# Kernel optimization log

Hardware: AMD Instinct MI355X
Metric: run time of the kernel (lower is better)

## Reference

```python
import jax, jax.numpy as jnp
import numpy as np

QUERY_DIM, FEAT_DIM, HID_DIM, OUT_DIM = 512, 2048, 512, 512
B, L, S, T = 8, 128, 100, 100


def setup_inputs() -> dict:
    key = jax.random.key(0)
    ks = jax.random.split(key, 9)
    d = {
        "query": jax.random.normal(ks[0], (B, L, QUERY_DIM), jnp.float32),
        "src": jax.random.normal(ks[1], (B, S, FEAT_DIM), jnp.float32),
        "trg": jax.random.normal(ks[2], (B, T, FEAT_DIM), jnp.float32),
        # params (LinearAct == Linear + identity act); src/trg projections share weights
        "Wq": jax.random.normal(ks[3], (QUERY_DIM, HID_DIM), jnp.float32) / np.sqrt(QUERY_DIM),
        "bq": jnp.zeros((HID_DIM,), jnp.float32),
        "Ws": jax.random.normal(ks[4], (FEAT_DIM, HID_DIM), jnp.float32) / np.sqrt(FEAT_DIM),
        "bs": jnp.zeros((HID_DIM,), jnp.float32),
        "Wo": jax.random.normal(ks[5], (HID_DIM + QUERY_DIM, OUT_DIM), jnp.float32) / np.sqrt(HID_DIM + QUERY_DIM),
        "bo": jnp.zeros((OUT_DIM,), jnp.float32),
    }
    return d


def reference(query, src, trg, Wq, bq, Ws, bs, Wo, bo):
    b, l, _ = query.shape
    s = src.shape[1]
    t = trg.shape[1]
    q = query @ Wq + bq          # b,l,k
    s_key = src @ Ws + bs        # b,s,k
    t_key = trg @ Ws + bs        # b,t,k
    hid = q.shape[-1]
    # score[b,l,s,t] = q . (s_key - t_key)/sqrt(2) / sqrt(hid) -- decomposed, no b,s,t,k tensor
    qs = jnp.einsum('blk,bsk->bls', q, s_key)
    qt = jnp.einsum('blk,btk->blt', q, t_key)
    score = (qs[:, :, :, None] - qt[:, :, None, :]) / jnp.sqrt(jnp.asarray(2.0 * hid, q.dtype))
    w = jax.nn.softmax(score.reshape(b, l, s * t), axis=-1).reshape(b, l, s, t)
    # ctx = sum_{s,t} w * (s_key - t_key)/sqrt(2), decomposed via marginals
    ws = w.sum(axis=3)           # b,l,s
    wt = w.sum(axis=2)           # b,l,t
    ctx = (jnp.einsum('bls,bsk->blk', ws, s_key) - jnp.einsum('blt,btk->blk', wt, t_key)) / jnp.sqrt(jnp.asarray(2.0, q.dtype))
    x = jnp.concatenate([query, ctx], axis=-1) @ Wo + bo
    return x
```

## Files before the change

### kernel.cpp

```cpp
#include <hip/hip_runtime.h>
#include <math.h>


typedef __attribute__((ext_vector_type(8))) short s16x8;
typedef __attribute__((ext_vector_type(4))) float f32x4;

__device__ __forceinline__ unsigned short f2bf(float f) {
    unsigned int u = __float_as_uint(f);
    return (unsigned short)((u + 0x7fffu + ((u >> 16) & 1u)) >> 16);
}

__device__ __forceinline__ s16x8 cvt8(const float* p) {
    float4 u = *(const float4*)p, w = *(const float4*)(p + 4);
    s16x8 o;
    o[0] = (short)f2bf(u.x); o[1] = (short)f2bf(u.y);
    o[2] = (short)f2bf(u.z); o[3] = (short)f2bf(u.w);
    o[4] = (short)f2bf(w.x); o[5] = (short)f2bf(w.y);
    o[6] = (short)f2bf(w.z); o[7] = (short)f2bf(w.w);
    return o;
}

__global__ __launch_bounds__(256) void k_prep(
    const float* __restrict__ Wq, const float* __restrict__ Ws,
    const float* __restrict__ Wo,
    unsigned short* __restrict__ WqT, unsigned short* __restrict__ WsT,
    unsigned short* __restrict__ WoT) {
    __shared__ float tile[32][33];
    const int id = blockIdx.x, t = threadIdx.x;

    const float* W; unsigned short* O; int K, tk, tn;
    if (id < 256)       { W = Wq; O = WqT; K = 512;  tk = id >> 4;          tn = id & 15; }
    else if (id < 1280) { W = Ws; O = WsT; K = 2048; tk = (id - 256) >> 4;  tn = (id - 256) & 15; }
    else                { W = Wo; O = WoT; K = 1024; tk = (id - 1280) >> 4; tn = (id - 1280) & 15; }
    const int row = t >> 3, c4 = (t & 7) * 4;
    float4 v = *(const float4*)(W + (size_t)(tk * 32 + row) * 512 + tn * 32 + c4);
    tile[row][c4 + 0] = v.x; tile[row][c4 + 1] = v.y;
    tile[row][c4 + 2] = v.z; tile[row][c4 + 3] = v.w;
    __syncthreads();
    ushort4 o = make_ushort4(f2bf(tile[c4 + 0][row]), f2bf(tile[c4 + 1][row]),
                             f2bf(tile[c4 + 2][row]), f2bf(tile[c4 + 3][row]));
    *(ushort4*)(O + (size_t)(tn * 32 + row) * K + tk * 32 + c4) = o;
}

__device__ __forceinline__ void gemm64_keys(
    const float* __restrict__ src, const float* __restrict__ trg,
    const unsigned short* __restrict__ BT, unsigned short* __restrict__ Kb,
    int m0, int n0, unsigned short* As, unsigned short* Bs) {
    const int t = threadIdx.x;
    const int lane = t & 63, wid = t >> 6;
    const int wm = (wid & 1) * 32, wn = (wid >> 1) * 32;
    const int lr = lane & 15, lq = lane >> 4;
    const int r = t >> 3, c8 = (t & 7) * 8;

    const int ra_row = m0 + r, rb_row = m0 + r + 32;
    const float* arp = (ra_row < 800) ? (src + (size_t)ra_row * 2048)
                                      : (trg + (size_t)(ra_row - 800) * 2048);
    const float* brp = (rb_row < 800) ? (src + (size_t)rb_row * 2048)
                                      : (trg + (size_t)(rb_row - 800) * 2048);

    s16x8 ra0, ra1, rb0, rb1;
#define LDK(kt)                                                            \
    ra0 = cvt8(arp + (kt) + c8);                                           \
    ra1 = cvt8(brp + (kt) + c8);                                           \
    rb0 = *(const s16x8*)(BT + (size_t)(n0 + r)      * 2048 + (kt) + c8);  \
    rb1 = *(const s16x8*)(BT + (size_t)(n0 + r + 32) * 2048 + (kt) + c8);

    f32x4 acc[2][2] = {};
    LDK(0);
    for (int it = 0; it < 32; it++) {
        __syncthreads();
        *(s16x8*)&As[r * 72 + c8]        = ra0;
        *(s16x8*)&As[(r + 32) * 72 + c8] = ra1;
        *(s16x8*)&Bs[r * 72 + c8]        = rb0;
        *(s16x8*)&Bs[(r + 32) * 72 + c8] = rb1;
        __syncthreads();
        if (it < 31) { LDK((it + 1) * 64); }
#pragma unroll
        for (int s = 0; s < 2; s++) {
            s16x8 a0 = *(const s16x8*)&As[(wm + lr) * 72      + s * 32 + lq * 8];
            s16x8 a1 = *(const s16x8*)&As[(wm + 16 + lr) * 72 + s * 32 + lq * 8];
            s16x8 b0 = *(const s16x8*)&Bs[(wn + lr) * 72      + s * 32 + lq * 8];
            s16x8 b1 = *(const s16x8*)&Bs[(wn + 16 + lr) * 72 + s * 32 + lq * 8];
            acc[0][0] = __builtin_amdgcn_mfma_f32_16x16x32_bf16(a0, b0, acc[0][0], 0, 0, 0);
            acc[0][1] = __builtin_amdgcn_mfma_f32_16x16x32_bf16(a0, b1, acc[0][1], 0, 0, 0);
            acc[1][0] = __builtin_amdgcn_mfma_f32_16x16x32_bf16(a1, b0, acc[1][0], 0, 0, 0);
            acc[1][1] = __builtin_amdgcn_mfma_f32_16x16x32_bf16(a1, b1, acc[1][1], 0, 0, 0);
        }
    }
#undef LDK
#pragma unroll
    for (int i = 0; i < 2; i++)
#pragma unroll
        for (int j = 0; j < 2; j++) {
            const int col = n0 + wn + j * 16 + lr;
            const int row = m0 + wm + i * 16 + lq * 4;
#pragma unroll
            for (int rr = 0; rr < 4; rr++)
                Kb[(size_t)(row + rr) * 512 + col] = f2bf(acc[i][j][rr]);
        }
}

__device__ __forceinline__ void gemm64_P(
    const unsigned short* __restrict__ Kb, const unsigned short* __restrict__ wotBot,
    float* __restrict__ P, int m0, int n0, unsigned short* As,
    unsigned short* Bs) {
    const int t = threadIdx.x;
    const int lane = t & 63, wid = t >> 6;
    const int wm = (wid & 1) * 32, wn = (wid >> 1) * 32;
    const int lr = lane & 15, lq = lane >> 4;
    const int r = t >> 3, c8 = (t & 7) * 8;

    s16x8 ra0, ra1, rb0, rb1;
#define LDP(kt)                                                               \
    ra0 = *(const s16x8*)(Kb + (size_t)(m0 + r)      * 512 + (kt) + c8);      \
    ra1 = *(const s16x8*)(Kb + (size_t)(m0 + r + 32) * 512 + (kt) + c8);      \
    rb0 = *(const s16x8*)(wotBot + (size_t)(n0 + r)      * 1024 + (kt) + c8); \
    rb1 = *(const s16x8*)(wotBot + (size_t)(n0 + r + 32) * 1024 + (kt) + c8);

    f32x4 acc[2][2] = {};
    LDP(0);
    for (int it = 0; it < 8; it++) {
        __syncthreads();
        *(s16x8*)&As[r * 72 + c8]        = ra0;
        *(s16x8*)&As[(r + 32) * 72 + c8] = ra1;
        *(s16x8*)&Bs[r * 72 + c8]        = rb0;
        *(s16x8*)&Bs[(r + 32) * 72 + c8] = rb1;
        __syncthreads();
        if (it < 7) { LDP((it + 1) * 64); }
#pragma unroll
        for (int s = 0; s < 2; s++) {
            s16x8 a0 = *(const s16x8*)&As[(wm + lr) * 72      + s * 32 + lq * 8];
            s16x8 a1 = *(const s16x8*)&As[(wm + 16 + lr) * 72 + s * 32 + lq * 8];
            s16x8 b0 = *(const s16x8*)&Bs[(wn + lr) * 72      + s * 32 + lq * 8];
            s16x8 b1 = *(const s16x8*)&Bs[(wn + 16 + lr) * 72 + s * 32 + lq * 8];
            acc[0][0] = __builtin_amdgcn_mfma_f32_16x16x32_bf16(a0, b0, acc[0][0], 0, 0, 0);
            acc[0][1] = __builtin_amdgcn_mfma_f32_16x16x32_bf16(a0, b1, acc[0][1], 0, 0, 0);
            acc[1][0] = __builtin_amdgcn_mfma_f32_16x16x32_bf16(a1, b0, acc[1][0], 0, 0, 0);
            acc[1][1] = __builtin_amdgcn_mfma_f32_16x16x32_bf16(a1, b1, acc[1][1], 0, 0, 0);
        }
    }
#undef LDP
#pragma unroll
    for (int i = 0; i < 2; i++)
#pragma unroll
        for (int j = 0; j < 2; j++) {
            const int col = n0 + wn + j * 16 + lr;
            const int row = m0 + wm + i * 16 + lq * 4;
#pragma unroll
            for (int rr = 0; rr < 4; rr++)
                P[(size_t)(row + rr) * 512 + col] = acc[i][j][rr];
        }
}

template <int MODE>
__device__ __forceinline__ void gemm32(
    const float* __restrict__ A, const unsigned short* __restrict__ BT,
    const float* __restrict__ bias, void* __restrict__ Cv,
    int m0, int n0, int KA, int KB, int N, int kiters,
    unsigned short* As, unsigned short* Bs) {
    const int t = threadIdx.x;
    const int lane = t & 63, wid = t >> 6;
    const int wm = (wid & 1) * 16, wn = (wid >> 1) * 32;
    const int lr = lane & 15, lq = lane >> 4;
    const int r = t >> 3, c8 = (t & 7) * 8;

    s16x8 ra, rb0, rb1;
#define LD32(kt)                                                            \
    ra  = cvt8(A + (size_t)(m0 + r) * KA + (kt) + c8);                      \
    rb0 = *(const s16x8*)(BT + (size_t)(n0 + r)      * KB + (kt) + c8);     \
    rb1 = *(const s16x8*)(BT + (size_t)(n0 + r + 32) * KB + (kt) + c8);

    f32x4 acc[2] = {};
    LD32(0);
    for (int it = 0; it < kiters; it++) {
        __syncthreads();
        *(s16x8*)&As[r * 72 + c8]        = ra;
        *(s16x8*)&Bs[r * 72 + c8]        = rb0;
        *(s16x8*)&Bs[(r + 32) * 72 + c8] = rb1;
        __syncthreads();
        if (it + 1 < kiters) { LD32((it + 1) * 64); }
#pragma unroll
        for (int s = 0; s < 2; s++) {
            s16x8 a0 = *(const s16x8*)&As[(wm + lr) * 72      + s * 32 + lq * 8];
            s16x8 b0 = *(const s16x8*)&Bs[(wn + lr) * 72      + s * 32 + lq * 8];
            s16x8 b1 = *(const s16x8*)&Bs[(wn + 16 + lr) * 72 + s * 32 + lq * 8];
            acc[0] = __builtin_amdgcn_mfma_f32_16x16x32_bf16(a0, b0, acc[0], 0, 0, 0);
            acc[1] = __builtin_amdgcn_mfma_f32_16x16x32_bf16(a0, b1, acc[1], 0, 0, 0);
        }
    }
#undef LD32
#pragma unroll
    for (int j = 0; j < 2; j++) {
        const int col = n0 + wn + j * 16 + lr;
        const int row = m0 + wm + lq * 4;
        const float bv = bias[col];
        if (MODE == 0) {
            float* C = (float*)Cv;
#pragma unroll
            for (int rr = 0; rr < 4; rr++)
                C[(size_t)(row + rr) * N + col] = acc[j][rr] + bv;
        } else {
            unsigned short* C = (unsigned short*)Cv;
#pragma unroll
            for (int rr = 0; rr < 4; rr++)
                C[(size_t)(row + rr) * N + col] = f2bf(acc[j][rr] + bv);
        }
    }
}

__global__ __launch_bounds__(256) void k_stageB(
    const float* __restrict__ query, const float* __restrict__ src,
    const float* __restrict__ trg, const unsigned short* __restrict__ WqT,
    const unsigned short* __restrict__ WsT, const unsigned short* __restrict__ WoT,
    const float* __restrict__ bq, const float* __restrict__ bo,
    unsigned short* __restrict__ qh, unsigned short* __restrict__ keysbf,
    float* __restrict__ out) {
    __shared__ __align__(16) unsigned short As[64 * 72];
    __shared__ __align__(16) unsigned short Bs[64 * 72];
    const int bid = blockIdx.x;
    if (bid < 200) {
        gemm64_keys(src, trg, WsT, keysbf, (bid >> 3) * 64, (bid & 7) * 64,
                    As, Bs);
    } else if (bid < 456) {
        const int r = bid - 200;
        gemm32<2>(query, WqT, bq, qh, (r >> 3) * 32, (r & 7) * 64, 512, 512,
                  512, 8, As, Bs);
    } else {
        const int r = bid - 456;
        gemm32<0>(query, WoT, bo, out, (r >> 3) * 32, (r & 7) * 64, 512, 1024,
                  512, 8, As, Bs);
    }
}

__global__ __launch_bounds__(256) void k_stageC(
    const unsigned short* __restrict__ qh, const unsigned short* __restrict__ keysbf,
    const unsigned short* __restrict__ wotBot, float* __restrict__ sc,
    float* __restrict__ P) {
    __shared__ __align__(16) unsigned short As[64 * 72];
    __shared__ __align__(16) unsigned short Bs[64 * 72];
    const int bid = blockIdx.x;
    const int t = threadIdx.x;

    if (bid >= 128) {
        const int rem = bid - 128;
        gemm64_P(keysbf, wotBot, P, (rem >> 3) * 64, (rem & 7) * 64, As, Bs);
        return;
    }

    const int mt = bid >> 2, nt = bid & 3;
    const int m0 = mt * 32, b = mt >> 2, n0 = nt * 64;
    const int lane = t & 63, wid = t >> 6;
    const int wm = (wid & 1) * 16, wn = (wid >> 1) * 32;
    const int lr = lane & 15, lq = lane >> 4;
    const int r = t >> 3, c8 = (t & 7) * 8;

    const int nA = n0 + r, nB = n0 + r + 32;
    int kr0 = (nA < 128) ? (b * 100 + nA) : (800 + b * 100 + (nA - 128));
    int kr1 = (nB < 128) ? (b * 100 + nB) : (800 + b * 100 + (nB - 128));
    kr0 = kr0 > 1599 ? 1599 : kr0;
    kr1 = kr1 > 1599 ? 1599 : kr1;

    s16x8 ra, rb0, rb1;
#define LDSC(kt)                                                        \
    ra  = *(const s16x8*)(qh + (size_t)(m0 + r) * 512 + (kt) + c8);     \
    rb0 = *(const s16x8*)(keysbf + (size_t)kr0 * 512 + (kt) + c8);      \
    rb1 = *(const s16x8*)(keysbf + (size_t)kr1 * 512 + (kt) + c8);

    f32x4 acc[2] = {};
    LDSC(0);
    for (int it = 0; it < 8; it++) {
        __syncthreads();
        *(s16x8*)&As[r * 72 + c8]        = ra;
        *(s16x8*)&Bs[r * 72 + c8]        = rb0;
        *(s16x8*)&Bs[(r + 32) * 72 + c8] = rb1;
        __syncthreads();
        if (it < 7) { LDSC((it + 1) * 64); }
#pragma unroll
        for (int s = 0; s < 2; s++) {
            s16x8 a0 = *(const s16x8*)&As[(wm + lr) * 72      + s * 32 + lq * 8];
            s16x8 b0 = *(const s16x8*)&Bs[(wn + lr) * 72      + s * 32 + lq * 8];
            s16x8 b1 = *(const s16x8*)&Bs[(wn + 16 + lr) * 72 + s * 32 + lq * 8];
            acc[0] = __builtin_amdgcn_mfma_f32_16x16x32_bf16(a0, b0, acc[0], 0, 0, 0);
            acc[1] = __builtin_amdgcn_mfma_f32_16x16x32_bf16(a0, b1, acc[1], 0, 0, 0);
        }
    }
#undef LDSC
#pragma unroll
    for (int j = 0; j < 2; j++) {
        const int col = n0 + wn + j * 16 + lr;
        const int row = m0 + wm + lq * 4;
        const float scale = (col >= 128) ? -(1.0f / 32.0f) : (1.0f / 32.0f);
#pragma unroll
        for (int rr = 0; rr < 4; rr++)
            sc[(size_t)(row + rr) * 256 + col] = acc[j][rr] * scale;
    }
}

__global__ __launch_bounds__(256) void k_stageD(
    const float* __restrict__ sc, const float* __restrict__ P,
    float* __restrict__ out) {
    __shared__ float wbuf[200 * 33];
    __shared__ float Bs[40 * 32];

    const int t = threadIdx.x;
    const int b = blockIdx.y;
    const int n0 = blockIdx.x * 32;
    const int l0 = blockIdx.z * 32;
    const int wave = t >> 6, lane = t & 63;

    for (int i = 0; i < 8; i++) {
        const int li = wave * 8 + i;
        const float4 v = *(const float4*)(
            sc + (size_t)(b * 128 + l0 + li) * 256 + lane * 4);
        const float vv[4] = {v.x, v.y, v.z, v.w};
        const int c0 = lane * 4;
        float mS = -1e30f, mT = -1e30f;
#pragma unroll
        for (int j = 0; j < 4; j++) {
            const int col = c0 + j;
            if (col < 100) mS = fmaxf(mS, vv[j]);
            if (col >= 128 && col < 228) mT = fmaxf(mT, vv[j]);
        }
#pragma unroll
        for (int off = 32; off > 0; off >>= 1) {
            mS = fmaxf(mS, __shfl_xor(mS, off));
            mT = fmaxf(mT, __shfl_xor(mT, off));
        }
        float eS[4], eT[4], sS = 0.f, sT = 0.f;
#pragma unroll
        for (int j = 0; j < 4; j++) {
            const int col = c0 + j;
            eS[j] = (col < 100) ? __expf(vv[j] - mS) : 0.f;
            eT[j] = (col >= 128 && col < 228) ? __expf(vv[j] - mT) : 0.f;
            sS += eS[j]; sT += eT[j];
        }
#pragma unroll
        for (int off = 32; off > 0; off >>= 1) {
            sS += __shfl_xor(sS, off);
            sT += __shfl_xor(sT, off);
        }
        const float iS = 1.f / sS, iT = 1.f / sT;
#pragma unroll
        for (int j = 0; j < 4; j++) {
            const int col = c0 + j;
            if (col < 100) wbuf[col * 33 + li] = eS[j] * iS;
            if (col >= 128 && col < 228)
                wbuf[(100 + col - 128) * 33 + li] = eT[j] * iT;
        }
    }
    __syncthreads();

    const int tx = t & 7, ty = t >> 3;
    float rB[5];
    auto loadB = [&](int kbase) {
#pragma unroll
        for (int e = 0; e < 5; e++) {
            const int idx = t + e * 256;
            const int k = idx >> 5, j = idx & 31;
            const int kk = kbase + k;
            rB[e] = (kk < 100)
                ?  P[(size_t)(b * 100 + kk) * 512 + n0 + j]
                : -P[(size_t)(800 + b * 100 + (kk - 100)) * 512 + n0 + j];
        }
    };

    float acc[4] = {};
    loadB(0);
    for (int c5 = 0; c5 < 5; c5++) {
        __syncthreads();
#pragma unroll
        for (int e = 0; e < 5; e++) {
            const int idx = t + e * 256;
            Bs[idx] = rB[e];
        }
        __syncthreads();
        if (c5 < 4) loadB((c5 + 1) * 40);
#pragma unroll 8
        for (int k = 0; k < 40; k++) {
            const float ar = wbuf[(c5 * 40 + k) * 33 + ty];
            float br[4];
            *(float4*)br = *(const float4*)&Bs[k * 32 + tx * 4];
#pragma unroll
            for (int j = 0; j < 4; j++) acc[j] = fmaf(ar, br[j], acc[j]);
        }
    }

    const float s2 = 0.70710678118654752f;
    const int m = b * 128 + l0 + ty;
#pragma unroll
    for (int j = 0; j < 4; j++)
        unsafeAtomicAdd(&out[(size_t)m * 512 + n0 + tx * 4 + j], acc[j] * s2);
}


extern "C" void kernel_launch(void* const* d_in, const int* in_sizes, int n_in,
                              void* d_out, int out_size, void* d_ws, size_t ws_size,
                              hipStream_t stream) {
    const float* query = (const float*)d_in[0];
    const float* src   = (const float*)d_in[1];
    const float* trg   = (const float*)d_in[2];
    const float* Wq    = (const float*)d_in[3];
    const float* bq    = (const float*)d_in[4];
    const float* Ws    = (const float*)d_in[5];
    const float* Wo    = (const float*)d_in[7];
    const float* bo    = (const float*)d_in[8];
    float* out = (float*)d_out;

    unsigned short* keysbf = (unsigned short*)d_ws;
    float* sc = (float*)(keysbf + 819200);
    float* P  = sc + 262144;
    unsigned short* qh  = (unsigned short*)(P + 819200);
    unsigned short* wqt = qh  + 524288;
    unsigned short* wst = wqt + 262144;
    unsigned short* wot = wst + 1048576;

    k_prep<<<1792, 256, 0, stream>>>(Wq, Ws, Wo, wqt, wst, wot);
    k_stageB<<<712, 256, 0, stream>>>(query, src, trg, wqt, wst, wot, bq, bo,
                                      qh, keysbf, out);
    k_stageC<<<328, 256, 0, stream>>>(qh, keysbf, wot + 512, sc, P);
    k_stageD<<<dim3(16, 8, 4), 256, 0, stream>>>(sc, P, out);
}
```

Before: 134.5 us.

## Fold Wq/Ws transpose-convert into GEMM loads and drop prep kernel

Removes the separate weight transpose/convert kernel for Wq and Ws. The keys and query GEMMs now read the fp32 weights directly with strided scalar loads and convert them to bf16 while staging into shared memory. The Wo transpose moves into the first stage as extra blocks, and the query@Wo_top GEMM moves to the second stage, so there is one fewer launch. The trade-off is uncoalesced column-strided loads of Ws (16 scalar loads per thread, repeated by every M-tile block) in place of a one-time transpose.

```diff
diff --git a/kernel.cpp b/kernel.cpp
--- a/kernel.cpp
+++ b/kernel.cpp
@@ -20,37 +20,16 @@
     return o;
 }
 
-__global__ __launch_bounds__(256) void k_prep(
-    const float* __restrict__ Wq, const float* __restrict__ Ws,
-    const float* __restrict__ Wo,
-    unsigned short* __restrict__ WqT, unsigned short* __restrict__ WsT,
-    unsigned short* __restrict__ WoT) {
-    __shared__ float tile[32][33];
-    const int id = blockIdx.x, t = threadIdx.x;
-
-    const float* W; unsigned short* O; int K, tk, tn;
-    if (id < 256)       { W = Wq; O = WqT; K = 512;  tk = id >> 4;          tn = id & 15; }
-    else if (id < 1280) { W = Ws; O = WsT; K = 2048; tk = (id - 256) >> 4;  tn = (id - 256) & 15; }
-    else                { W = Wo; O = WoT; K = 1024; tk = (id - 1280) >> 4; tn = (id - 1280) & 15; }
-    const int row = t >> 3, c4 = (t & 7) * 4;
-    float4 v = *(const float4*)(W + (size_t)(tk * 32 + row) * 512 + tn * 32 + c4);
-    tile[row][c4 + 0] = v.x; tile[row][c4 + 1] = v.y;
-    tile[row][c4 + 2] = v.z; tile[row][c4 + 3] = v.w;
-    __syncthreads();
-    ushort4 o = make_ushort4(f2bf(tile[c4 + 0][row]), f2bf(tile[c4 + 1][row]),
-                             f2bf(tile[c4 + 2][row]), f2bf(tile[c4 + 3][row]));
-    *(ushort4*)(O + (size_t)(tn * 32 + row) * K + tk * 32 + c4) = o;
-}
-
 __device__ __forceinline__ void gemm64_keys(
     const float* __restrict__ src, const float* __restrict__ trg,
-    const unsigned short* __restrict__ BT, unsigned short* __restrict__ Kb,
+    const float* __restrict__ Ws, unsigned short* __restrict__ Kb,
     int m0, int n0, unsigned short* As, unsigned short* Bs) {
     const int t = threadIdx.x;
     const int lane = t & 63, wid = t >> 6;
     const int wm = (wid & 1) * 32, wn = (wid >> 1) * 32;
     const int lr = lane & 15, lq = lane >> 4;
     const int r = t >> 3, c8 = (t & 7) * 8;
+    const int nrow = t >> 2, kc16 = (t & 3) * 16;
 
     const int ra_row = m0 + r, rb_row = m0 + r + 32;
     const float* arp = (ra_row < 800) ? (src + (size_t)ra_row * 2048)
@@ -58,12 +37,14 @@
     const float* brp = (rb_row < 800) ? (src + (size_t)rb_row * 2048)
                                       : (trg + (size_t)(rb_row - 800) * 2048);
 
-    s16x8 ra0, ra1, rb0, rb1;
-#define LDK(kt)                                                            \
-    ra0 = cvt8(arp + (kt) + c8);                                           \
-    ra1 = cvt8(brp + (kt) + c8);                                           \
-    rb0 = *(const s16x8*)(BT + (size_t)(n0 + r)      * 2048 + (kt) + c8);  \
-    rb1 = *(const s16x8*)(BT + (size_t)(n0 + r + 32) * 2048 + (kt) + c8);
+    s16x8 ra0, ra1;
+    float bw[16];
+#define LDK(kt)                                                              \
+    ra0 = cvt8(arp + (kt) + c8);                                             \
+    ra1 = cvt8(brp + (kt) + c8);                                             \
+    _Pragma("unroll")                                                        \
+    for (int j = 0; j < 16; j++)                                             \
+        bw[j] = Ws[(size_t)((kt) + kc16 + j) * 512 + n0 + nrow];
 
     f32x4 acc[2][2] = {};
     LDK(0);
@@ -71,8 +52,16 @@
         __syncthreads();
         *(s16x8*)&As[r * 72 + c8]        = ra0;
         *(s16x8*)&As[(r + 32) * 72 + c8] = ra1;
-        *(s16x8*)&Bs[r * 72 + c8]        = rb0;
-        *(s16x8*)&Bs[(r + 32) * 72 + c8] = rb1;
+        {
+            s16x8 bb0, bb1;
+#pragma unroll
+            for (int j = 0; j < 8; j++) {
+                bb0[j] = (short)f2bf(bw[j]);
+                bb1[j] = (short)f2bf(bw[8 + j]);
+            }
+            *(s16x8*)&Bs[nrow * 72 + kc16]     = bb0;
+            *(s16x8*)&Bs[nrow * 72 + kc16 + 8] = bb1;
+        }
         __syncthreads();
         if (it < 31) { LDK((it + 1) * 64); }
 #pragma unroll
@@ -100,6 +89,109 @@
         }
 }
 
+__device__ __forceinline__ void gemm32_rawB(
+    const float* __restrict__ A, const float* __restrict__ W,
+    const float* __restrict__ bias, unsigned short* __restrict__ C,
+    int m0, int n0, unsigned short* As, unsigned short* Bs) {
+    const int t = threadIdx.x;
+    const int lane = t & 63, wid = t >> 6;
+    const int wm = (wid & 1) * 16, wn = (wid >> 1) * 32;
+    const int lr = lane & 15, lq = lane >> 4;
+    const int r = t >> 3, c8 = (t & 7) * 8;
+    const int nrow = t >> 2, kc16 = (t & 3) * 16;
+
+    s16x8 ra;
+    float bw[16];
+#define LDQ(kt)                                                              \
+    ra = cvt8(A + (size_t)(m0 + r) * 512 + (kt) + c8);                       \
+    _Pragma("unroll")                                                        \
+    for (int j = 0; j < 16; j++)                                             \
+        bw[j] = W[(size_t)((kt) + kc16 + j) * 512 + n0 + nrow];
+
+    f32x4 acc[2] = {};
+    LDQ(0);
+    for (int it = 0; it < 8; it++) {
+        __syncthreads();
+        *(s16x8*)&As[r * 72 + c8] = ra;
+        {
+            s16x8 bb0, bb1;
+#pragma unroll
+            for (int j = 0; j < 8; j++) {
+                bb0[j] = (short)f2bf(bw[j]);
+                bb1[j] = (short)f2bf(bw[8 + j]);
+            }
+            *(s16x8*)&Bs[nrow * 72 + kc16]     = bb0;
+            *(s16x8*)&Bs[nrow * 72 + kc16 + 8] = bb1;
+        }
+        __syncthreads();
+        if (it < 7) { LDQ((it + 1) * 64); }
+#pragma unroll
+        for (int s = 0; s < 2; s++) {
+            s16x8 a0 = *(const s16x8*)&As[(wm + lr) * 72      + s * 32 + lq * 8];
+            s16x8 b0 = *(const s16x8*)&Bs[(wn + lr) * 72      + s * 32 + lq * 8];
+            s16x8 b1 = *(const s16x8*)&Bs[(wn + 16 + lr) * 72 + s * 32 + lq * 8];
+            acc[0] = __builtin_amdgcn_mfma_f32_16x16x32_bf16(a0, b0, acc[0], 0, 0, 0);
+            acc[1] = __builtin_amdgcn_mfma_f32_16x16x32_bf16(a0, b1, acc[1], 0, 0, 0);
+        }
+    }
+#undef LDQ
+#pragma unroll
+    for (int j = 0; j < 2; j++) {
+        const int col = n0 + wn + j * 16 + lr;
+        const int row = m0 + wm + lq * 4;
+        const float bv = bias[col];
+#pragma unroll
+        for (int rr = 0; rr < 4; rr++)
+            C[(size_t)(row + rr) * 512 + col] = f2bf(acc[j][rr] + bv);
+    }
+}
+
+__device__ __forceinline__ void gemm32_cvtA(
+    const float* __restrict__ A, const unsigned short* __restrict__ BT,
+    const float* __restrict__ bias, float* __restrict__ C,
+    int m0, int n0, int KB, unsigned short* As, unsigned short* Bs) {
+    const int t = threadIdx.x;
+    const int lane = t & 63, wid = t >> 6;
+    const int wm = (wid & 1) * 16, wn = (wid >> 1) * 32;
+    const int lr = lane & 15, lq = lane >> 4;
+    const int r = t >> 3, c8 = (t & 7) * 8;
+
+    s16x8 ra, rb0, rb1;
+#define LD32(kt)                                                            \
+    ra  = cvt8(A + (size_t)(m0 + r) * 512 + (kt) + c8);                     \
+    rb0 = *(const s16x8*)(BT + (size_t)(n0 + r)      * KB + (kt) + c8);     \
+    rb1 = *(const s16x8*)(BT + (size_t)(n0 + r + 32) * KB + (kt) + c8);
+
+    f32x4 acc[2] = {};
+    LD32(0);
+    for (int it = 0; it < 8; it++) {
+        __syncthreads();
+        *(s16x8*)&As[r * 72 + c8]        = ra;
+        *(s16x8*)&Bs[r * 72 + c8]        = rb0;
+        *(s16x8*)&Bs[(r + 32) * 72 + c8] = rb1;
+        __syncthreads();
+        if (it < 7) { LD32((it + 1) * 64); }
+#pragma unroll
+        for (int s = 0; s < 2; s++) {
+            s16x8 a0 = *(const s16x8*)&As[(wm + lr) * 72      + s * 32 + lq * 8];
+            s16x8 b0 = *(const s16x8*)&Bs[(wn + lr) * 72      + s * 32 + lq * 8];
+            s16x8 b1 = *(const s16x8*)&Bs[(wn + 16 + lr) * 72 + s * 32 + lq * 8];
+            acc[0] = __builtin_amdgcn_mfma_f32_16x16x32_bf16(a0, b0, acc[0], 0, 0, 0);
+            acc[1] = __builtin_amdgcn_mfma_f32_16x16x32_bf16(a0, b1, acc[1], 0, 0, 0);
+        }
+    }
+#undef LD32
+#pragma unroll
+    for (int j = 0; j < 2; j++) {
+        const int col = n0 + wn + j * 16 + lr;
+        const int row = m0 + wm + lq * 4;
+        const float bv = bias[col];
+#pragma unroll
+        for (int rr = 0; rr < 4; rr++)
+            C[(size_t)(row + rr) * 512 + col] = acc[j][rr] + bv;
+    }
+}
+
 __device__ __forceinline__ void gemm64_P(
     const unsigned short* __restrict__ Kb, const unsigned short* __restrict__ wotBot,
     float* __restrict__ P, int m0, int n0, unsigned short* As,
@@ -152,98 +244,56 @@
         }
 }
 
-template <int MODE>
-__device__ __forceinline__ void gemm32(
-    const float* __restrict__ A, const unsigned short* __restrict__ BT,
-    const float* __restrict__ bias, void* __restrict__ Cv,
-    int m0, int n0, int KA, int KB, int N, int kiters,
-    unsigned short* As, unsigned short* Bs) {
-    const int t = threadIdx.x;
-    const int lane = t & 63, wid = t >> 6;
-    const int wm = (wid & 1) * 16, wn = (wid >> 1) * 32;
-    const int lr = lane & 15, lq = lane >> 4;
-    const int r = t >> 3, c8 = (t & 7) * 8;
-
-    s16x8 ra, rb0, rb1;
-#define LD32(kt)                                                            \
-    ra  = cvt8(A + (size_t)(m0 + r) * KA + (kt) + c8);                      \
-    rb0 = *(const s16x8*)(BT + (size_t)(n0 + r)      * KB + (kt) + c8);     \
-    rb1 = *(const s16x8*)(BT + (size_t)(n0 + r + 32) * KB + (kt) + c8);
-
-    f32x4 acc[2] = {};
-    LD32(0);
-    for (int it = 0; it < kiters; it++) {
-        __syncthreads();
-        *(s16x8*)&As[r * 72 + c8]        = ra;
-        *(s16x8*)&Bs[r * 72 + c8]        = rb0;
-        *(s16x8*)&Bs[(r + 32) * 72 + c8] = rb1;
-        __syncthreads();
-        if (it + 1 < kiters) { LD32((it + 1) * 64); }
-#pragma unroll
-        for (int s = 0; s < 2; s++) {
-            s16x8 a0 = *(const s16x8*)&As[(wm + lr) * 72      + s * 32 + lq * 8];
-            s16x8 b0 = *(const s16x8*)&Bs[(wn + lr) * 72      + s * 32 + lq * 8];
-            s16x8 b1 = *(const s16x8*)&Bs[(wn + 16 + lr) * 72 + s * 32 + lq * 8];
-            acc[0] = __builtin_amdgcn_mfma_f32_16x16x32_bf16(a0, b0, acc[0], 0, 0, 0);
-            acc[1] = __builtin_amdgcn_mfma_f32_16x16x32_bf16(a0, b1, acc[1], 0, 0, 0);
-        }
-    }
-#undef LD32
-#pragma unroll
-    for (int j = 0; j < 2; j++) {
-        const int col = n0 + wn + j * 16 + lr;
-        const int row = m0 + wm + lq * 4;
-        const float bv = bias[col];
-        if (MODE == 0) {
-            float* C = (float*)Cv;
-#pragma unroll
-            for (int rr = 0; rr < 4; rr++)
-                C[(size_t)(row + rr) * N + col] = acc[j][rr] + bv;
-        } else {
-            unsigned short* C = (unsigned short*)Cv;
-#pragma unroll
-            for (int rr = 0; rr < 4; rr++)
-                C[(size_t)(row + rr) * N + col] = f2bf(acc[j][rr] + bv);
-        }
-    }
-}
-
-__global__ __launch_bounds__(256) void k_stageB(
+__global__ __launch_bounds__(256) void k_stage1(
     const float* __restrict__ query, const float* __restrict__ src,
-    const float* __restrict__ trg, const unsigned short* __restrict__ WqT,
-    const unsigned short* __restrict__ WsT, const unsigned short* __restrict__ WoT,
-    const float* __restrict__ bq, const float* __restrict__ bo,
-    unsigned short* __restrict__ qh, unsigned short* __restrict__ keysbf,
-    float* __restrict__ out) {
+    const float* __restrict__ trg, const float* __restrict__ Wq,
+    const float* __restrict__ Ws, const float* __restrict__ Wo,
+    const float* __restrict__ bq, unsigned short* __restrict__ qh,
+    unsigned short* __restrict__ keysbf, unsigned short* __restrict__ wot) {
+    __shared__ __align__(16) unsigned short As[64 * 72];
+    __shared__ __align__(16) unsigned short Bs[64 * 72];
+    const int bid = blockIdx.x, t = threadIdx.x;
+
+    if (bid < 200) {
+        gemm64_keys(src, trg, Ws, keysbf, (bid >> 3) * 64, (bid & 7) * 64,
+                    As, Bs);
+    } else if (bid < 456) {
+        const int rr = bid - 200;
+        gemm32_rawB(query, Wq, bq, qh, (rr >> 3) * 32, (rr & 7) * 64, As, Bs);
+    } else {
+        float (*tile)[33] = (float(*)[33])As;
+        const int id2 = bid - 456;
+        const int tk = id2 >> 4, tn = id2 & 15;
+        const int row = t >> 3, c4 = (t & 7) * 4;
+        float4 v = *(const float4*)(Wo + (size_t)(tk * 32 + row) * 512 + tn * 32 + c4);
+        tile[row][c4 + 0] = v.x; tile[row][c4 + 1] = v.y;
+        tile[row][c4 + 2] = v.z; tile[row][c4 + 3] = v.w;
+        __syncthreads();
+        ushort4 o = make_ushort4(f2bf(tile[c4 + 0][row]), f2bf(tile[c4 + 1][row]),
+                                 f2bf(tile[c4 + 2][row]), f2bf(tile[c4 + 3][row]));
+        *(ushort4*)(wot + (size_t)(tn * 32 + row) * 1024 + tk * 32 + c4) = o;
+    }
+}
+
+__global__ __launch_bounds__(256) void k_stage2(
+    const float* __restrict__ query, const unsigned short* __restrict__ qh,
+    const unsigned short* __restrict__ keysbf,
+    const unsigned short* __restrict__ wot, const float* __restrict__ bo,
+    float* __restrict__ sc, float* __restrict__ P, float* __restrict__ out) {
     __shared__ __align__(16) unsigned short As[64 * 72];
     __shared__ __align__(16) unsigned short Bs[64 * 72];
     const int bid = blockIdx.x;
-    if (bid < 200) {
-        gemm64_keys(src, trg, WsT, keysbf, (bid >> 3) * 64, (bid & 7) * 64,
+    const int t = threadIdx.x;
+
+    if (bid >= 328) {
+        const int rr = bid - 328;
+        gemm32_cvtA(query, wot, bo, out, (rr >> 3) * 32, (rr & 7) * 64, 1024,
                     As, Bs);
-    } else if (bid < 456) {
-        const int r = bid - 200;
-        gemm32<2>(query, WqT, bq, qh, (r >> 3) * 32, (r & 7) * 64, 512, 512,
-                  512, 8, As, Bs);
-    } else {
-        const int r = bid - 456;
-        gemm32<0>(query, WoT, bo, out, (r >> 3) * 32, (r & 7) * 64, 512, 1024,
-                  512, 8, As, Bs);
-    }
-}
-
-__global__ __launch_bounds__(256) void k_stageC(
-    const unsigned short* __restrict__ qh, const unsigned short* __restrict__ keysbf,
-    const unsigned short* __restrict__ wotBot, float* __restrict__ sc,
-    float* __restrict__ P) {
-    __shared__ __align__(16) unsigned short As[64 * 72];
-    __shared__ __align__(16) unsigned short Bs[64 * 72];
-    const int bid = blockIdx.x;
-    const int t = threadIdx.x;
-
+        return;
+    }
     if (bid >= 128) {
         const int rem = bid - 128;
-        gemm64_P(keysbf, wotBot, P, (rem >> 3) * 64, (rem & 7) * 64, As, Bs);
+        gemm64_P(keysbf, wot + 512, P, (rem >> 3) * 64, (rem & 7) * 64, As, Bs);
         return;
     }
 
@@ -410,13 +460,10 @@
     float* sc = (float*)(keysbf + 819200);
     float* P  = sc + 262144;
     unsigned short* qh  = (unsigned short*)(P + 819200);
-    unsigned short* wqt = qh  + 524288;
-    unsigned short* wst = wqt + 262144;
-    unsigned short* wot = wst + 1048576;
-
-    k_prep<<<1792, 256, 0, stream>>>(Wq, Ws, Wo, wqt, wst, wot);
-    k_stageB<<<712, 256, 0, stream>>>(query, src, trg, wqt, wst, wot, bq, bo,
-                                      qh, keysbf, out);
-    k_stageC<<<328, 256, 0, stream>>>(qh, keysbf, wot + 512, sc, P);
+    unsigned short* wot = qh + 524288;
+
+    k_stage1<<<968, 256, 0, stream>>>(query, src, trg, Wq, Ws, Wo, bq,
+                                      qh, keysbf, wot);
+    k_stage2<<<584, 256, 0, stream>>>(query, qh, keysbf, wot, bo, sc, P, out);
     k_stageD<<<dim3(16, 8, 4), 256, 0, stream>>>(sc, P, out);
 }
```

After: 153.4 us. 14.0% more time.

## Split-K the key projection GEMM with atomics and rebalance stage work

Applied to the files above, without the earlier changes.

The src/trg key projection (K=2048) is split four ways across blocks, with fp32 atomic accumulation into a keys buffer that is zeroed in the prep kernel. Keys are now stored in fp32 and converted to bf16 when loaded in stage C. The Wo transpose moves into stage B and the query@Wo output GEMM moves into stage C, so both stages get more parallel work. The costs are atomic traffic, twice the key storage bandwidth, and nondeterministic summation order.

```diff
diff --git a/kernel.cpp b/kernel.cpp
--- a/kernel.cpp
+++ b/kernel.cpp
@@ -22,30 +22,33 @@
 
 __global__ __launch_bounds__(256) void k_prep(
     const float* __restrict__ Wq, const float* __restrict__ Ws,
-    const float* __restrict__ Wo,
     unsigned short* __restrict__ WqT, unsigned short* __restrict__ WsT,
-    unsigned short* __restrict__ WoT) {
+    float* __restrict__ keys) {
     __shared__ float tile[32][33];
     const int id = blockIdx.x, t = threadIdx.x;
 
-    const float* W; unsigned short* O; int K, tk, tn;
-    if (id < 256)       { W = Wq; O = WqT; K = 512;  tk = id >> 4;          tn = id & 15; }
-    else if (id < 1280) { W = Ws; O = WsT; K = 2048; tk = (id - 256) >> 4;  tn = (id - 256) & 15; }
-    else                { W = Wo; O = WoT; K = 1024; tk = (id - 1280) >> 4; tn = (id - 1280) & 15; }
-    const int row = t >> 3, c4 = (t & 7) * 4;
-    float4 v = *(const float4*)(W + (size_t)(tk * 32 + row) * 512 + tn * 32 + c4);
-    tile[row][c4 + 0] = v.x; tile[row][c4 + 1] = v.y;
-    tile[row][c4 + 2] = v.z; tile[row][c4 + 3] = v.w;
-    __syncthreads();
-    ushort4 o = make_ushort4(f2bf(tile[c4 + 0][row]), f2bf(tile[c4 + 1][row]),
-                             f2bf(tile[c4 + 2][row]), f2bf(tile[c4 + 3][row]));
-    *(ushort4*)(O + (size_t)(tn * 32 + row) * K + tk * 32 + c4) = o;
+    if (id < 1280) {
+        const float* W; unsigned short* O; int K, tk, tn;
+        if (id < 256) { W = Wq; O = WqT; K = 512;  tk = id >> 4;         tn = id & 15; }
+        else          { W = Ws; O = WsT; K = 2048; tk = (id - 256) >> 4; tn = (id - 256) & 15; }
+        const int row = t >> 3, c4 = (t & 7) * 4;
+        float4 v = *(const float4*)(W + (size_t)(tk * 32 + row) * 512 + tn * 32 + c4);
+        tile[row][c4 + 0] = v.x; tile[row][c4 + 1] = v.y;
+        tile[row][c4 + 2] = v.z; tile[row][c4 + 3] = v.w;
+        __syncthreads();
+        ushort4 o = make_ushort4(f2bf(tile[c4 + 0][row]), f2bf(tile[c4 + 1][row]),
+                                 f2bf(tile[c4 + 2][row]), f2bf(tile[c4 + 3][row]));
+        *(ushort4*)(O + (size_t)(tn * 32 + row) * K + tk * 32 + c4) = o;
+    } else {
+        const int f = ((id - 1280) * 256 + t) * 4;
+        *(float4*)(keys + f) = make_float4(0.f, 0.f, 0.f, 0.f);
+    }
 }
 
 __device__ __forceinline__ void gemm64_keys(
     const float* __restrict__ src, const float* __restrict__ trg,
-    const unsigned short* __restrict__ BT, unsigned short* __restrict__ Kb,
-    int m0, int n0, unsigned short* As, unsigned short* Bs) {
+    const unsigned short* __restrict__ BT, float* __restrict__ Kf,
+    int m0, int n0, int kbase, unsigned short* As, unsigned short* Bs) {
     const int t = threadIdx.x;
     const int lane = t & 63, wid = t >> 6;
     const int wm = (wid & 1) * 32, wn = (wid >> 1) * 32;
@@ -66,15 +69,15 @@
     rb1 = *(const s16x8*)(BT + (size_t)(n0 + r + 32) * 2048 + (kt) + c8);
 
     f32x4 acc[2][2] = {};
-    LDK(0);
-    for (int it = 0; it < 32; it++) {
+    LDK(kbase);
+    for (int it = 0; it < 8; it++) {
         __syncthreads();
         *(s16x8*)&As[r * 72 + c8]        = ra0;
         *(s16x8*)&As[(r + 32) * 72 + c8] = ra1;
         *(s16x8*)&Bs[r * 72 + c8]        = rb0;
         *(s16x8*)&Bs[(r + 32) * 72 + c8] = rb1;
         __syncthreads();
-        if (it < 31) { LDK((it + 1) * 64); }
+        if (it < 7) { LDK(kbase + (it + 1) * 64); }
 #pragma unroll
         for (int s = 0; s < 2; s++) {
             s16x8 a0 = *(const s16x8*)&As[(wm + lr) * 72      + s * 32 + lq * 8];
@@ -96,59 +99,8 @@
             const int row = m0 + wm + i * 16 + lq * 4;
 #pragma unroll
             for (int rr = 0; rr < 4; rr++)
-                Kb[(size_t)(row + rr) * 512 + col] = f2bf(acc[i][j][rr]);
-        }
-}
-
-__device__ __forceinline__ void gemm64_P(
-    const unsigned short* __restrict__ Kb, const unsigned short* __restrict__ wotBot,
-    float* __restrict__ P, int m0, int n0, unsigned short* As,
-    unsigned short* Bs) {
-    const int t = threadIdx.x;
-    const int lane = t & 63, wid = t >> 6;
-    const int wm = (wid & 1) * 32, wn = (wid >> 1) * 32;
-    const int lr = lane & 15, lq = lane >> 4;
-    const int r = t >> 3, c8 = (t & 7) * 8;
-
-    s16x8 ra0, ra1, rb0, rb1;
-#define LDP(kt)                                                               \
-    ra0 = *(const s16x8*)(Kb + (size_t)(m0 + r)      * 512 + (kt) + c8);      \
-    ra1 = *(const s16x8*)(Kb + (size_t)(m0 + r + 32) * 512 + (kt) + c8);      \
-    rb0 = *(const s16x8*)(wotBot + (size_t)(n0 + r)      * 1024 + (kt) + c8); \
-    rb1 = *(const s16x8*)(wotBot + (size_t)(n0 + r + 32) * 1024 + (kt) + c8);
-
-    f32x4 acc[2][2] = {};
-    LDP(0);
-    for (int it = 0; it < 8; it++) {
-        __syncthreads();
-        *(s16x8*)&As[r * 72 + c8]        = ra0;
-        *(s16x8*)&As[(r + 32) * 72 + c8] = ra1;
-        *(s16x8*)&Bs[r * 72 + c8]        = rb0;
-        *(s16x8*)&Bs[(r + 32) * 72 + c8] = rb1;
-        __syncthreads();
-        if (it < 7) { LDP((it + 1) * 64); }
-#pragma unroll
-        for (int s = 0; s < 2; s++) {
-            s16x8 a0 = *(const s16x8*)&As[(wm + lr) * 72      + s * 32 + lq * 8];
-            s16x8 a1 = *(const s16x8*)&As[(wm + 16 + lr) * 72 + s * 32 + lq * 8];
-            s16x8 b0 = *(const s16x8*)&Bs[(wn + lr) * 72      + s * 32 + lq * 8];
-            s16x8 b1 = *(const s16x8*)&Bs[(wn + 16 + lr) * 72 + s * 32 + lq * 8];
-            acc[0][0] = __builtin_amdgcn_mfma_f32_16x16x32_bf16(a0, b0, acc[0][0], 0, 0, 0);
-            acc[0][1] = __builtin_amdgcn_mfma_f32_16x16x32_bf16(a0, b1, acc[0][1], 0, 0, 0);
-            acc[1][0] = __builtin_amdgcn_mfma_f32_16x16x32_bf16(a1, b0, acc[1][0], 0, 0, 0);
-            acc[1][1] = __builtin_amdgcn_mfma_f32_16x16x32_bf16(a1, b1, acc[1][1], 0, 0, 0);
-        }
-    }
-#undef LDP
-#pragma unroll
-    for (int i = 0; i < 2; i++)
-#pragma unroll
-        for (int j = 0; j < 2; j++) {
-            const int col = n0 + wn + j * 16 + lr;
-            const int row = m0 + wm + i * 16 + lq * 4;
-#pragma unroll
-            for (int rr = 0; rr < 4; rr++)
-                P[(size_t)(row + rr) * 512 + col] = acc[i][j][rr];
+                unsafeAtomicAdd(&Kf[(size_t)(row + rr) * 512 + col],
+                                acc[i][j][rr]);
         }
 }
 
@@ -208,42 +160,110 @@
     }
 }
 
+__device__ __forceinline__ void gemm64_P(
+    const float* __restrict__ Kf, const unsigned short* __restrict__ wotBot,
+    float* __restrict__ P, int m0, int n0, unsigned short* As,
+    unsigned short* Bs) {
+    const int t = threadIdx.x;
+    const int lane = t & 63, wid = t >> 6;
+    const int wm = (wid & 1) * 32, wn = (wid >> 1) * 32;
+    const int lr = lane & 15, lq = lane >> 4;
+    const int r = t >> 3, c8 = (t & 7) * 8;
+
+    s16x8 ra0, ra1, rb0, rb1;
+#define LDP(kt)                                                               \
+    ra0 = cvt8(Kf + (size_t)(m0 + r)      * 512 + (kt) + c8);                 \
+    ra1 = cvt8(Kf + (size_t)(m0 + r + 32) * 512 + (kt) + c8);                 \
+    rb0 = *(const s16x8*)(wotBot + (size_t)(n0 + r)      * 1024 + (kt) + c8); \
+    rb1 = *(const s16x8*)(wotBot + (size_t)(n0 + r + 32) * 1024 + (kt) + c8);
+
+    f32x4 acc[2][2] = {};
+    LDP(0);
+    for (int it = 0; it < 8; it++) {
+        __syncthreads();
+        *(s16x8*)&As[r * 72 + c8]        = ra0;
+        *(s16x8*)&As[(r + 32) * 72 + c8] = ra1;
+        *(s16x8*)&Bs[r * 72 + c8]        = rb0;
+        *(s16x8*)&Bs[(r + 32) * 72 + c8] = rb1;
+        __syncthreads();
+        if (it < 7) { LDP((it + 1) * 64); }
+#pragma unroll
+        for (int s = 0; s < 2; s++) {
+            s16x8 a0 = *(const s16x8*)&As[(wm + lr) * 72      + s * 32 + lq * 8];
+            s16x8 a1 = *(const s16x8*)&As[(wm + 16 + lr) * 72 + s * 32 + lq * 8];
+            s16x8 b0 = *(const s16x8*)&Bs[(wn + lr) * 72      + s * 32 + lq * 8];
+            s16x8 b1 = *(const s16x8*)&Bs[(wn + 16 + lr) * 72 + s * 32 + lq * 8];
+            acc[0][0] = __builtin_amdgcn_mfma_f32_16x16x32_bf16(a0, b0, acc[0][0], 0, 0, 0);
+            acc[0][1] = __builtin_amdgcn_mfma_f32_16x16x32_bf16(a0, b1, acc[0][1], 0, 0, 0);
+            acc[1][0] = __builtin_amdgcn_mfma_f32_16x16x32_bf16(a1, b0, acc[1][0], 0, 0, 0);
+            acc[1][1] = __builtin_amdgcn_mfma_f32_16x16x32_bf16(a1, b1, acc[1][1], 0, 0, 0);
+        }
+    }
+#undef LDP
+#pragma unroll
+    for (int i = 0; i < 2; i++)
+#pragma unroll
+        for (int j = 0; j < 2; j++) {
+            const int col = n0 + wn + j * 16 + lr;
+            const int row = m0 + wm + i * 16 + lq * 4;
+#pragma unroll
+            for (int rr = 0; rr < 4; rr++)
+                P[(size_t)(row + rr) * 512 + col] = acc[i][j][rr];
+        }
+}
+
 __global__ __launch_bounds__(256) void k_stageB(
     const float* __restrict__ query, const float* __restrict__ src,
-    const float* __restrict__ trg, const unsigned short* __restrict__ WqT,
-    const unsigned short* __restrict__ WsT, const unsigned short* __restrict__ WoT,
-    const float* __restrict__ bq, const float* __restrict__ bo,
-    unsigned short* __restrict__ qh, unsigned short* __restrict__ keysbf,
-    float* __restrict__ out) {
+    const float* __restrict__ trg, const unsigned short* __restrict__ wqt,
+    const unsigned short* __restrict__ wst, const float* __restrict__ Wo,
+    const float* __restrict__ bq, unsigned short* __restrict__ qh,
+    float* __restrict__ keys, unsigned short* __restrict__ wot) {
     __shared__ __align__(16) unsigned short As[64 * 72];
     __shared__ __align__(16) unsigned short Bs[64 * 72];
-    const int bid = blockIdx.x;
-    if (bid < 200) {
-        gemm64_keys(src, trg, WsT, keysbf, (bid >> 3) * 64, (bid & 7) * 64,
-                    As, Bs);
-    } else if (bid < 456) {
-        const int r = bid - 200;
-        gemm32<2>(query, WqT, bq, qh, (r >> 3) * 32, (r & 7) * 64, 512, 512,
-                  512, 8, As, Bs);
+    const int bid = blockIdx.x, t = threadIdx.x;
+
+    if (bid < 800) {
+        const int c = bid / 200, rem = bid % 200;
+        gemm64_keys(src, trg, wst, keys, (rem >> 3) * 64, (rem & 7) * 64,
+                    c * 512, As, Bs);
+    } else if (bid < 1056) {
+        const int rr = bid - 800;
+        gemm32<2>(query, wqt, bq, qh, (rr >> 3) * 32, (rr & 7) * 64,
+                  512, 512, 512, 8, As, Bs);
     } else {
-        const int r = bid - 456;
-        gemm32<0>(query, WoT, bo, out, (r >> 3) * 32, (r & 7) * 64, 512, 1024,
-                  512, 8, As, Bs);
+        float (*tile)[33] = (float(*)[33])As;
+        const int id2 = bid - 1056;
+        const int tk = id2 >> 4, tn = id2 & 15;
+        const int row = t >> 3, c4 = (t & 7) * 4;
+        float4 v = *(const float4*)(Wo + (size_t)(tk * 32 + row) * 512 + tn * 32 + c4);
+        tile[row][c4 + 0] = v.x; tile[row][c4 + 1] = v.y;
+        tile[row][c4 + 2] = v.z; tile[row][c4 + 3] = v.w;
+        __syncthreads();
+        ushort4 o = make_ushort4(f2bf(tile[c4 + 0][row]), f2bf(tile[c4 + 1][row]),
+                                 f2bf(tile[c4 + 2][row]), f2bf(tile[c4 + 3][row]));
+        *(ushort4*)(wot + (size_t)(tn * 32 + row) * 1024 + tk * 32 + c4) = o;
     }
 }
 
 __global__ __launch_bounds__(256) void k_stageC(
-    const unsigned short* __restrict__ qh, const unsigned short* __restrict__ keysbf,
-    const unsigned short* __restrict__ wotBot, float* __restrict__ sc,
-    float* __restrict__ P) {
+    const float* __restrict__ query, const unsigned short* __restrict__ qh,
+    const float* __restrict__ keys, const unsigned short* __restrict__ wot,
+    const float* __restrict__ bo, float* __restrict__ sc,
+    float* __restrict__ P, float* __restrict__ out) {
     __shared__ __align__(16) unsigned short As[64 * 72];
     __shared__ __align__(16) unsigned short Bs[64 * 72];
     const int bid = blockIdx.x;
     const int t = threadIdx.x;
 
+    if (bid >= 328) {
+        const int rr = bid - 328;
+        gemm32<0>(query, wot, bo, out, (rr >> 3) * 32, (rr & 7) * 64,
+                  512, 1024, 512, 8, As, Bs);
+        return;
+    }
     if (bid >= 128) {
         const int rem = bid - 128;
-        gemm64_P(keysbf, wotBot, P, (rem >> 3) * 64, (rem & 7) * 64, As, Bs);
+        gemm64_P(keys, wot + 512, P, (rem >> 3) * 64, (rem & 7) * 64, As, Bs);
         return;
     }
 
@@ -263,8 +283,8 @@
     s16x8 ra, rb0, rb1;
 #define LDSC(kt)                                                        \
     ra  = *(const s16x8*)(qh + (size_t)(m0 + r) * 512 + (kt) + c8);     \
-    rb0 = *(const s16x8*)(keysbf + (size_t)kr0 * 512 + (kt) + c8);      \
-    rb1 = *(const s16x8*)(keysbf + (size_t)kr1 * 512 + (kt) + c8);
+    rb0 = cvt8(keys + (size_t)kr0 * 512 + (kt) + c8);                   \
+    rb1 = cvt8(keys + (size_t)kr1 * 512 + (kt) + c8);
 
     f32x4 acc[2] = {};
     LDSC(0);
@@ -406,17 +426,17 @@
     const float* bo    = (const float*)d_in[8];
     float* out = (float*)d_out;
 
-    unsigned short* keysbf = (unsigned short*)d_ws;
-    float* sc = (float*)(keysbf + 819200);
-    float* P  = sc + 262144;
+    float* keys = (float*)d_ws;
+    float* sc   = keys + 819200;
+    float* P    = sc + 262144;
     unsigned short* qh  = (unsigned short*)(P + 819200);
-    unsigned short* wqt = qh  + 524288;
+    unsigned short* wqt = qh + 524288;
     unsigned short* wst = wqt + 262144;
     unsigned short* wot = wst + 1048576;
 
-    k_prep<<<1792, 256, 0, stream>>>(Wq, Ws, Wo, wqt, wst, wot);
-    k_stageB<<<712, 256, 0, stream>>>(query, src, trg, wqt, wst, wot, bq, bo,
-                                      qh, keysbf, out);
-    k_stageC<<<328, 256, 0, stream>>>(qh, keysbf, wot + 512, sc, P);
+    k_prep<<<2080, 256, 0, stream>>>(Wq, Ws, wqt, wst, keys);
+    k_stageB<<<1568, 256, 0, stream>>>(query, src, trg, wqt, wst, Wo, bq,
+                                       qh, keys, wot);
+    k_stageC<<<584, 256, 0, stream>>>(query, qh, keys, wot, bo, sc, P, out);
     k_stageD<<<dim3(16, 8, 4), 256, 0, stream>>>(sc, P, out);
 }
```

Result: no change. 136.7 us (+1.6%).

## Split-K the key projection GEMM in two with fp32 atomic accumulation

Applied to the files above, without the earlier changes.

The src/trg key projection (K=2048) now runs as two K-halves per output tile, which doubles its block count, and the partial sums are accumulated into an fp32 keys buffer with atomics. The prep kernel gains extra blocks that zero this buffer. Downstream stages now read fp32 keys and convert them to bf16 on load. This targets the long serial K loop and the low block count of the key GEMM. In exchange it adds atomic traffic, twice the keys storage and read bandwidth, and makes the accumulation order nondeterministic.

```diff
diff --git a/kernel.cpp b/kernel.cpp
--- a/kernel.cpp
+++ b/kernel.cpp
@@ -24,28 +24,34 @@
     const float* __restrict__ Wq, const float* __restrict__ Ws,
     const float* __restrict__ Wo,
     unsigned short* __restrict__ WqT, unsigned short* __restrict__ WsT,
-    unsigned short* __restrict__ WoT) {
+    unsigned short* __restrict__ WoT, float* __restrict__ keys) {
     __shared__ float tile[32][33];
-    const int id = blockIdx.x, t = threadIdx.x;
-
-    const float* W; unsigned short* O; int K, tk, tn;
-    if (id < 256)       { W = Wq; O = WqT; K = 512;  tk = id >> 4;          tn = id & 15; }
-    else if (id < 1280) { W = Ws; O = WsT; K = 2048; tk = (id - 256) >> 4;  tn = (id - 256) & 15; }
-    else                { W = Wo; O = WoT; K = 1024; tk = (id - 1280) >> 4; tn = (id - 1280) & 15; }
-    const int row = t >> 3, c4 = (t & 7) * 4;
-    float4 v = *(const float4*)(W + (size_t)(tk * 32 + row) * 512 + tn * 32 + c4);
-    tile[row][c4 + 0] = v.x; tile[row][c4 + 1] = v.y;
-    tile[row][c4 + 2] = v.z; tile[row][c4 + 3] = v.w;
-    __syncthreads();
-    ushort4 o = make_ushort4(f2bf(tile[c4 + 0][row]), f2bf(tile[c4 + 1][row]),
-                             f2bf(tile[c4 + 2][row]), f2bf(tile[c4 + 3][row]));
-    *(ushort4*)(O + (size_t)(tn * 32 + row) * K + tk * 32 + c4) = o;
+    const int bid = blockIdx.x, t = threadIdx.x;
+
+    if (bid < 1792) {
+        const int id = bid;
+        const float* W; unsigned short* O; int K, tk, tn;
+        if (id < 256)       { W = Wq; O = WqT; K = 512;  tk = id >> 4;          tn = id & 15; }
+        else if (id < 1280) { W = Ws; O = WsT; K = 2048; tk = (id - 256) >> 4;  tn = (id - 256) & 15; }
+        else                { W = Wo; O = WoT; K = 1024; tk = (id - 1280) >> 4; tn = (id - 1280) & 15; }
+        const int row = t >> 3, c4 = (t & 7) * 4;
+        float4 v = *(const float4*)(W + (size_t)(tk * 32 + row) * 512 + tn * 32 + c4);
+        tile[row][c4 + 0] = v.x; tile[row][c4 + 1] = v.y;
+        tile[row][c4 + 2] = v.z; tile[row][c4 + 3] = v.w;
+        __syncthreads();
+        ushort4 o = make_ushort4(f2bf(tile[c4 + 0][row]), f2bf(tile[c4 + 1][row]),
+                                 f2bf(tile[c4 + 2][row]), f2bf(tile[c4 + 3][row]));
+        *(ushort4*)(O + (size_t)(tn * 32 + row) * K + tk * 32 + c4) = o;
+    } else {
+        const int f = ((bid - 1792) * 256 + t) * 4;
+        *(float4*)(keys + f) = make_float4(0.f, 0.f, 0.f, 0.f);
+    }
 }
 
 __device__ __forceinline__ void gemm64_keys(
     const float* __restrict__ src, const float* __restrict__ trg,
-    const unsigned short* __restrict__ BT, unsigned short* __restrict__ Kb,
-    int m0, int n0, unsigned short* As, unsigned short* Bs) {
+    const unsigned short* __restrict__ BT, float* __restrict__ C,
+    int m0, int n0, int kbase, unsigned short* As, unsigned short* Bs) {
     const int t = threadIdx.x;
     const int lane = t & 63, wid = t >> 6;
     const int wm = (wid & 1) * 32, wn = (wid >> 1) * 32;
@@ -66,15 +72,15 @@
     rb1 = *(const s16x8*)(BT + (size_t)(n0 + r + 32) * 2048 + (kt) + c8);
 
     f32x4 acc[2][2] = {};
-    LDK(0);
-    for (int it = 0; it < 32; it++) {
+    LDK(kbase);
+    for (int it = 0; it < 16; it++) {
         __syncthreads();
         *(s16x8*)&As[r * 72 + c8]        = ra0;
         *(s16x8*)&As[(r + 32) * 72 + c8] = ra1;
         *(s16x8*)&Bs[r * 72 + c8]        = rb0;
         *(s16x8*)&Bs[(r + 32) * 72 + c8] = rb1;
         __syncthreads();
-        if (it < 31) { LDK((it + 1) * 64); }
+        if (it < 15) { LDK(kbase + (it + 1) * 64); }
 #pragma unroll
         for (int s = 0; s < 2; s++) {
             s16x8 a0 = *(const s16x8*)&As[(wm + lr) * 72      + s * 32 + lq * 8];
@@ -96,12 +102,12 @@
             const int row = m0 + wm + i * 16 + lq * 4;
 #pragma unroll
             for (int rr = 0; rr < 4; rr++)
-                Kb[(size_t)(row + rr) * 512 + col] = f2bf(acc[i][j][rr]);
+                unsafeAtomicAdd(&C[(size_t)(row + rr) * 512 + col], acc[i][j][rr]);
         }
 }
 
 __device__ __forceinline__ void gemm64_P(
-    const unsigned short* __restrict__ Kb, const unsigned short* __restrict__ wotBot,
+    const float* __restrict__ keys, const unsigned short* __restrict__ wotBot,
     float* __restrict__ P, int m0, int n0, unsigned short* As,
     unsigned short* Bs) {
     const int t = threadIdx.x;
@@ -112,8 +118,8 @@
 
     s16x8 ra0, ra1, rb0, rb1;
 #define LDP(kt)                                                               \
-    ra0 = *(const s16x8*)(Kb + (size_t)(m0 + r)      * 512 + (kt) + c8);      \
-    ra1 = *(const s16x8*)(Kb + (size_t)(m0 + r + 32) * 512 + (kt) + c8);      \
+    ra0 = cvt8(keys + (size_t)(m0 + r)      * 512 + (kt) + c8);               \
+    ra1 = cvt8(keys + (size_t)(m0 + r + 32) * 512 + (kt) + c8);               \
     rb0 = *(const s16x8*)(wotBot + (size_t)(n0 + r)      * 1024 + (kt) + c8); \
     rb1 = *(const s16x8*)(wotBot + (size_t)(n0 + r + 32) * 1024 + (kt) + c8);
 
@@ -213,27 +219,30 @@
     const float* __restrict__ trg, const unsigned short* __restrict__ WqT,
     const unsigned short* __restrict__ WsT, const unsigned short* __restrict__ WoT,
     const float* __restrict__ bq, const float* __restrict__ bo,
-    unsigned short* __restrict__ qh, unsigned short* __restrict__ keysbf,
+    unsigned short* __restrict__ qh, float* __restrict__ keys,
     float* __restrict__ out) {
     __shared__ __align__(16) unsigned short As[64 * 72];
     __shared__ __align__(16) unsigned short Bs[64 * 72];
     const int bid = blockIdx.x;
-    if (bid < 200) {
-        gemm64_keys(src, trg, WsT, keysbf, (bid >> 3) * 64, (bid & 7) * 64,
-                    As, Bs);
-    } else if (bid < 456) {
-        const int r = bid - 200;
-        gemm32<2>(query, WqT, bq, qh, (r >> 3) * 32, (r & 7) * 64, 512, 512,
-                  512, 8, As, Bs);
+    if (bid < 400) {
+        const int c = bid / 200, rem = bid % 200;
+        const int mt = rem >> 3, nt = rem & 7;
+        gemm64_keys(src, trg, WsT, keys, mt * 64, nt * 64, c * 1024, As, Bs);
+    } else if (bid < 656) {
+        const int r = bid - 400;
+        const int mt = r >> 3, nt = r & 7;
+        gemm32<2>(query, WqT, bq, qh, mt * 32, nt * 64, 512, 512, 512,
+                  8, As, Bs);
     } else {
-        const int r = bid - 456;
-        gemm32<0>(query, WoT, bo, out, (r >> 3) * 32, (r & 7) * 64, 512, 1024,
-                  512, 8, As, Bs);
+        const int r = bid - 656;
+        const int mt = r >> 3, nt = r & 7;
+        gemm32<0>(query, WoT, bo, out, mt * 32, nt * 64, 512, 1024, 512,
+                  8, As, Bs);
     }
 }
 
 __global__ __launch_bounds__(256) void k_stageC(
-    const unsigned short* __restrict__ qh, const unsigned short* __restrict__ keysbf,
+    const unsigned short* __restrict__ qh, const float* __restrict__ keys,
     const unsigned short* __restrict__ wotBot, float* __restrict__ sc,
     float* __restrict__ P) {
     __shared__ __align__(16) unsigned short As[64 * 72];
@@ -243,7 +252,7 @@
 
     if (bid >= 128) {
         const int rem = bid - 128;
-        gemm64_P(keysbf, wotBot, P, (rem >> 3) * 64, (rem & 7) * 64, As, Bs);
+        gemm64_P(keys, wotBot, P, (rem >> 3) * 64, (rem & 7) * 64, As, Bs);
         return;
     }
 
@@ -261,10 +270,10 @@
     kr1 = kr1 > 1599 ? 1599 : kr1;
 
     s16x8 ra, rb0, rb1;
-#define LDSC(kt)                                                        \
-    ra  = *(const s16x8*)(qh + (size_t)(m0 + r) * 512 + (kt) + c8);     \
-    rb0 = *(const s16x8*)(keysbf + (size_t)kr0 * 512 + (kt) + c8);      \
-    rb1 = *(const s16x8*)(keysbf + (size_t)kr1 * 512 + (kt) + c8);
+#define LDSC(kt)                                                    \
+    ra  = *(const s16x8*)(qh + (size_t)(m0 + r) * 512 + (kt) + c8); \
+    rb0 = cvt8(keys + (size_t)kr0 * 512 + (kt) + c8);               \
+    rb1 = cvt8(keys + (size_t)kr1 * 512 + (kt) + c8);
 
     f32x4 acc[2] = {};
     LDSC(0);
@@ -406,17 +415,17 @@
     const float* bo    = (const float*)d_in[8];
     float* out = (float*)d_out;
 
-    unsigned short* keysbf = (unsigned short*)d_ws;
-    float* sc = (float*)(keysbf + 819200);
-    float* P  = sc + 262144;
+    float* keys = (float*)d_ws;
+    float* sc   = keys + 819200;
+    float* P    = sc   + 262144;
     unsigned short* qh  = (unsigned short*)(P + 819200);
     unsigned short* wqt = qh  + 524288;
     unsigned short* wst = wqt + 262144;
     unsigned short* wot = wst + 1048576;
 
-    k_prep<<<1792, 256, 0, stream>>>(Wq, Ws, Wo, wqt, wst, wot);
-    k_stageB<<<712, 256, 0, stream>>>(query, src, trg, wqt, wst, wot, bq, bo,
-                                      qh, keysbf, out);
-    k_stageC<<<328, 256, 0, stream>>>(qh, keysbf, wot + 512, sc, P);
+    k_prep<<<2592, 256, 0, stream>>>(Wq, Ws, Wo, wqt, wst, wot, keys);
+    k_stageB<<<912, 256, 0, stream>>>(query, src, trg, wqt, wst, wot, bq, bo,
+                                      qh, keys, out);
+    k_stageC<<<328, 256, 0, stream>>>(qh, keys, wot + 512, sc, P);
     k_stageD<<<dim3(16, 8, 4), 256, 0, stream>>>(sc, P, out);
 }
```

Result: faster. 130.7 us (-2.9%).
